# Optimization experiments

Hardware: AMD Instinct MI355X
Metric: run time of the kernel (lower is better)

## Reference

```python
import jax, jax.numpy as jnp
import numpy as np

BN_EPS = 1e-5

def _haar_details(x):
    # pywt.dwt2(x, 'haar') details for even H, W.
    # Block [[p, q], [r, s]] with p = x[2i,2j], q = x[2i,2j+1], r = x[2i+1,2j], s = x[2i+1,2j+1].
    # cH ('da'): detail along rows, approx along cols; cV ('ad'); cD ('dd').
    B, C, H, W = x.shape
    xb = x.reshape(B, C, H // 2, 2, W // 2, 2)
    p = xb[:, :, :, 0, :, 0]
    q = xb[:, :, :, 0, :, 1]
    r = xb[:, :, :, 1, :, 0]
    s = xb[:, :, :, 1, :, 1]
    cH = (p + q - r - s) * 0.5
    cV = (p - q + r - s) * 0.5
    cD = (p - q - r + s) * 0.5
    return cH, cV, cD

def setup_inputs() -> dict:
    key = jax.random.key(0)
    k1, k2 = jax.random.split(key)
    B, C, H, W = 8, 256, 128, 128
    x = jax.random.normal(k1, (B, C, H, W), dtype=jnp.float32)
    conv_w = jax.random.normal(k2, (C, 4 * C), dtype=jnp.float32) * (1.0 / np.sqrt(4 * C))
    gamma = jnp.ones((C,), dtype=jnp.float32)
    beta = jnp.zeros((C,), dtype=jnp.float32)
    return {"x": x, "conv_w": conv_w, "gamma": gamma, "beta": beta}

def reference(x, conv_w, gamma, beta):
    B, C, H, W = x.shape
    # Original detaches the wavelet branch (CPU numpy path) -> stop_gradient.
    xs = jax.lax.stop_gradient(x)
    cH, cV, cD = _haar_details(xs)
    # Bilinear upsample to (H, W); jax.image.resize bilinear == torch align_corners=False.
    up = lambda t: jax.image.resize(t, (B, C, H, W), method="bilinear")
    enhanced = jnp.concatenate([x, up(cH), up(cV), up(cD)], axis=1)  # [B, 4C, H, W]
    # 1x1 conv, no bias.
    y = jnp.einsum("bchw,oc->bohw", enhanced, conv_w)  # [B, C, H, W]
    # BatchNorm2d, training-mode (batch statistics, biased variance).
    mean = jnp.mean(y, axis=(0, 2, 3), keepdims=True)
    var = jnp.mean((y - mean) ** 2, axis=(0, 2, 3), keepdims=True)
    y_hat = (y - mean) * jax.lax.rsqrt(var + BN_EPS)
    out = jax.nn.relu(y_hat * gamma[None, :, None, None] + beta[None, :, None, None])
    return out
```

## Files before the change

### kernel.cpp

```cpp
#include <hip/hip_runtime.h>
#include <hip/hip_bf16.h>

typedef __bf16 bf16;
typedef __bf16 bf16x4 __attribute__((ext_vector_type(4)));
typedef __bf16 bf16x8 __attribute__((ext_vector_type(8)));
typedef float  f32x4  __attribute__((ext_vector_type(4)));

#define AS1 __attribute__((address_space(1)))
#define AS3 __attribute__((address_space(3)))

__device__ __forceinline__ void load16_to_lds(const bf16* g, bf16* l) {
    __builtin_amdgcn_global_load_lds((const AS1 unsigned int*)g,
                                     (AS3 unsigned int*)l, 16, 0, 0);
}

__global__ __launch_bounds__(256) void prep_w(const float* __restrict__ w,
                                              bf16* __restrict__ wb) {
    int idx = (blockIdx.x * 256 + threadIdx.x) * 4;
    const float4 v = *(const float4*)(w + idx);
    bf16x4 o; o[0]=(bf16)v.x; o[1]=(bf16)v.y; o[2]=(bf16)v.z; o[3]=(bf16)v.w;
    *(bf16x4*)(wb + idx) = o;
}

__device__ __forceinline__ int tix(int row, int chunk, int lo) {
    return row * 264 + (((chunk ^ ((row >> 2) & 7)) << 3) | lo);
}

__global__ __launch_bounds__(256, 2) void fused_x(const float* __restrict__ x,
                                                  const bf16* __restrict__ W,
                                                  bf16* __restrict__ cT,
                                                  bf16* __restrict__ y1) {
    __shared__ bf16 tile[64 * 264];
    const int bid = blockIdx.x;
    const int wt = bid & 3, j = (bid >> 2) & 63, b = bid >> 8;
    const int t = threadIdx.x;
    const int w0 = wt * 32;
    const int wave = t >> 6, lane = t & 63;
    const int quad = lane >> 4, l16 = lane & 15;
    const int wo = wave * 64;

    #pragma unroll
    for (int half = 0; half < 2; ++half) {
        float4 v[8];
        #pragma unroll
        for (int i = 0; i < 8; ++i) {
            int g = (half * 8 + i) * 256 + t;
            int c = g >> 4, rem = g & 15;
            int dlt = rem >> 3, w4 = rem & 7;
            v[i] = *(const float4*)(x +
                ((((size_t)b * 256 + c) * 128 + (2 * j + dlt)) * 128 + w0 + w4 * 4));
        }
        #pragma unroll
        for (int i = 0; i < 8; ++i) {
            int g = (half * 8 + i) * 256 + t;
            int c = g >> 4, rem = g & 15;
            int dlt = rem >> 3, w4 = rem & 7;
            int pos = dlt * 32 + w4 * 4;
            int cs = tix(pos, c >> 3, c & 7) - pos * 264;
            tile[(pos + 0) * 264 + cs] = (bf16)v[i].x;
            tile[(pos + 1) * 264 + cs] = (bf16)v[i].y;
            tile[(pos + 2) * 264 + cs] = (bf16)v[i].z;
            tile[(pos + 3) * 264 + cs] = (bf16)v[i].w;
        }
    }

    bf16x8 wf_cur[4], wf_nxt[4];
    #pragma unroll
    for (int jj = 0; jj < 4; ++jj)
        wf_cur[jj] = *(const bf16x8*)(W +
            (size_t)(wo + jj * 16 + l16) * 1024 + quad * 8);

    __syncthreads();

    #pragma unroll
    for (int i = 0; i < 2; ++i) {
        int q = i * 256 + t;
        int cq = q & 31, kc = q >> 5;
        bf16x8 vp = *(const bf16x8*)&tile[tix(2 * kc, cq, 0)];
        bf16x8 vq = *(const bf16x8*)&tile[tix(2 * kc + 1, cq, 0)];
        bf16x8 vr = *(const bf16x8*)&tile[tix(32 + 2 * kc, cq, 0)];
        bf16x8 vs = *(const bf16x8*)&tile[tix(33 + 2 * kc, cq, 0)];
        bf16x8 oh, ov, od;
        #pragma unroll
        for (int e = 0; e < 8; ++e) {
            float p = (float)vp[e], qq = (float)vq[e];
            float r = (float)vr[e], s = (float)vs[e];
            oh[e] = (bf16)(0.5f * (p + qq - r - s));
            ov[e] = (bf16)(0.5f * (p - qq + r - s));
            od[e] = (bf16)(0.5f * (p - qq - r + s));
        }
        size_t row = ((size_t)b * 4096 + j * 64 + wt * 16 + kc) * 768;
        *(bf16x8*)(cT + row + 0 * 256 + cq * 8) = oh;
        *(bf16x8*)(cT + row + 1 * 256 + cq * 8) = ov;
        *(bf16x8*)(cT + row + 2 * 256 + cq * 8) = od;
    }

    f32x4 acc[4][4] = {};
    #pragma unroll
    for (int kk = 0; kk < 256; kk += 32) {
        if (kk < 224) {
            #pragma unroll
            for (int jj = 0; jj < 4; ++jj)
                wf_nxt[jj] = *(const bf16x8*)(W +
                    (size_t)(wo + jj * 16 + l16) * 1024 + kk + 32 + quad * 8);
        }
        bf16x8 xf[4];
        #pragma unroll
        for (int i2 = 0; i2 < 4; ++i2)
            xf[i2] = *(const bf16x8*)&tile[tix(i2 * 16 + l16,
                                               (kk >> 3) + quad, 0)];
        #pragma unroll
        for (int i2 = 0; i2 < 4; ++i2)
            #pragma unroll
            for (int jj = 0; jj < 4; ++jj)
                acc[i2][jj] = __builtin_amdgcn_mfma_f32_16x16x32_bf16(
                    xf[i2], wf_cur[jj], acc[i2][jj], 0, 0, 0);
        #pragma unroll
        for (int jj = 0; jj < 4; ++jj) wf_cur[jj] = wf_nxt[jj];
    }

    #pragma unroll
    for (int i = 0; i < 4; ++i) {
        int p = i * 16 + quad * 4;
        int h = 2 * j + (p >> 5), wc = w0 + (p & 31);
        #pragma unroll
        for (int jj = 0; jj < 4; ++jj) {
            int o = wo + jj * 16 + l16;
            bf16x4 vv;
            #pragma unroll
            for (int r = 0; r < 4; ++r) vv[r] = (bf16)acc[i][jj][r];
            *(bf16x4*)(y1 + ((size_t)b * 256 + o) * 16384 + h * 128 + wc) = vv;
        }
    }
}

__global__ __launch_bounds__(256) void gemm2(const bf16* __restrict__ W,
                                             const bf16* __restrict__ cT,
                                             bf16* __restrict__ z) {
    __shared__ bf16 Xt[128 * 32];
    const int bid = blockIdx.x;
    const int m0 = (bid & 255) * 128, o0 = (bid >> 8) * 128;
    const int t = threadIdx.x;
    const int wave = t >> 6, lane = t & 63;
    const int quad = lane >> 4, l16 = lane & 15;
    const int wo = (wave >> 1) * 64, wm = (wave & 1) * 64;
    const int r_in = lane >> 2, cch = lane & 3;

    f32x4 acc[4][4] = {};
    const bf16* wbase = W + (size_t)o0 * 1024 + 256;
    const bf16* xbase = cT + (size_t)m0 * 768;

    bf16x8 af_cur[4], af_nxt[4];
    #pragma unroll
    for (int i = 0; i < 4; ++i)
        af_cur[i] = *(const bf16x8*)(wbase +
            (size_t)(wo + i * 16 + l16) * 1024 + quad * 8);

    for (int kk = 0; kk < 768; kk += 32) {
        #pragma unroll
        for (int i = 0; i < 2; ++i) {
            int rblk = wave * 2 + i;
            int row = rblk * 16 + r_in;
            load16_to_lds(xbase + (size_t)row * 768 + kk + cch * 8,
                          &Xt[rblk * 512 + lane * 8]);
        }
        __syncthreads();
        if (kk < 736) {
            #pragma unroll
            for (int i = 0; i < 4; ++i)
                af_nxt[i] = *(const bf16x8*)(wbase +
                    (size_t)(wo + i * 16 + l16) * 1024 + kk + 32 + quad * 8);
        }
        bf16x8 bfr[4];
        #pragma unroll
        for (int jj = 0; jj < 4; ++jj)
            bfr[jj] = *(const bf16x8*)&Xt[(wm + jj * 16 + l16) * 32 + quad * 8];
        #pragma unroll
        for (int i = 0; i < 4; ++i)
            #pragma unroll
            for (int jj = 0; jj < 4; ++jj)
                acc[i][jj] = __builtin_amdgcn_mfma_f32_16x16x32_bf16(
                    bfr[jj], af_cur[i], acc[i][jj], 0, 0, 0);
        __syncthreads();
        #pragma unroll
        for (int i = 0; i < 4; ++i) af_cur[i] = af_nxt[i];
    }

    #pragma unroll
    for (int i = 0; i < 4; ++i) {
        int o = o0 + wo + i * 16 + l16;
        #pragma unroll
        for (int jj = 0; jj < 4; ++jj) {
            int m = m0 + wm + jj * 16 + quad * 4;
            int bb = m >> 12, mp = m & 4095;
            bf16x4 vv;
            #pragma unroll
            for (int r = 0; r < 4; ++r) vv[r] = (bf16)acc[i][jj][r];
            *(bf16x4*)(z + ((size_t)bb * 256 + o) * 4096 + mp) = vv;
        }
    }
}

__device__ __forceinline__ void load_zplane(const bf16* zp, float* zs, int t) {
    for (int i = 0; i < 2; ++i) {
        int idx = (i * 256 + t) * 8;
        int j = idx >> 6, k = idx & 63;
        bf16x8 v = *(const bf16x8*)(zp + idx);
        #pragma unroll
        for (int e = 0; e < 8; ++e) zs[j * 65 + k + e] = (float)v[e];
    }
}

__device__ __forceinline__ void up8(const float* zs, int base, float* u) {
    int h = base >> 7, w0 = base & 127;
    int j0 = h >> 1;
    int jn = (h & 1) ? min(j0 + 1, 63) : max(j0 - 1, 0);
    int K = w0 >> 1;
    float z0[6], z1[6];
    #pragma unroll
    for (int d = 0; d < 6; ++d) {
        int kc = min(max(K - 1 + d, 0), 63);
        z0[d] = zs[j0 * 65 + kc];
        z1[d] = zs[jn * 65 + kc];
    }
    #pragma unroll
    for (int e = 0; e < 8; ++e) {
        int a = (e >> 1) + 1;
        int bb = (e & 1) ? a + 1 : a - 1;
        u[e] = 0.5625f * z0[a] + 0.1875f * (z0[bb] + z1[a]) + 0.0625f * z1[bb];
    }
}

__global__ __launch_bounds__(256) void stats_k(const bf16* __restrict__ y1,
                                               const bf16* __restrict__ z,
                                               float* __restrict__ stats) {
    __shared__ float zs[64 * 65];
    __shared__ float red[8];
    const int bid = blockIdx.x;
    const int o = bid & 255, b = bid >> 8;
    const int t = threadIdx.x;
    const bf16* zp = z + ((size_t)b * 256 + o) * 4096;
    const bf16* yp = y1 + ((size_t)b * 256 + o) * 16384;
    load_zplane(zp, zs, t);
    __syncthreads();
    float s = 0.f, ss = 0.f;
    for (int i = 0; i < 8; ++i) {
        int base = (i * 256 + t) * 8;
        float u[8];
        up8(zs, base, u);
        bf16x8 yv = *(const bf16x8*)(yp + base);
        #pragma unroll
        for (int e = 0; e < 8; ++e) {
            float y = (float)yv[e] + u[e];
            s += y; ss += y * y;
        }
    }
    #pragma unroll
    for (int off = 32; off > 0; off >>= 1) {
        s += __shfl_down(s, off);
        ss += __shfl_down(ss, off);
    }
    if ((t & 63) == 0) { red[t >> 6] = s; red[4 + (t >> 6)] = ss; }
    __syncthreads();
    if (t == 0) {
        atomicAdd(&stats[o],       red[0] + red[1] + red[2] + red[3]);
        atomicAdd(&stats[256 + o], red[4] + red[5] + red[6] + red[7]);
    }
}

__global__ __launch_bounds__(256) void apply_k(const bf16* __restrict__ y1,
                                               const bf16* __restrict__ z,
                                               const float* __restrict__ stats,
                                               const float* __restrict__ gamma,
                                               const float* __restrict__ beta,
                                               float* __restrict__ out) {
    __shared__ float zs[64 * 65];
    const int bid = blockIdx.x;
    const int o = bid & 255, b = bid >> 8;
    const int t = threadIdx.x;
    const bf16* zp = z + ((size_t)b * 256 + o) * 4096;
    const bf16* yp = y1 + ((size_t)b * 256 + o) * 16384;
    float* op = out + ((size_t)b * 256 + o) * 16384;
    const float n = 131072.f;
    float mean = stats[o] / n;
    float var = stats[256 + o] / n - mean * mean;
    float sc = rsqrtf(var + 1e-5f) * gamma[o];
    float sh = beta[o] - mean * sc;
    load_zplane(zp, zs, t);
    __syncthreads();
    for (int i = 0; i < 8; ++i) {
        int base = (i * 256 + t) * 8;
        float u[8];
        up8(zs, base, u);
        bf16x8 yv = *(const bf16x8*)(yp + base);
        float4 o0, o1;
        o0.x = fmaxf(fmaf((float)yv[0] + u[0], sc, sh), 0.f);
        o0.y = fmaxf(fmaf((float)yv[1] + u[1], sc, sh), 0.f);
        o0.z = fmaxf(fmaf((float)yv[2] + u[2], sc, sh), 0.f);
        o0.w = fmaxf(fmaf((float)yv[3] + u[3], sc, sh), 0.f);
        o1.x = fmaxf(fmaf((float)yv[4] + u[4], sc, sh), 0.f);
        o1.y = fmaxf(fmaf((float)yv[5] + u[5], sc, sh), 0.f);
        o1.z = fmaxf(fmaf((float)yv[6] + u[6], sc, sh), 0.f);
        o1.w = fmaxf(fmaf((float)yv[7] + u[7], sc, sh), 0.f);
        *(float4*)(op + base) = o0;
        *(float4*)(op + base + 4) = o1;
    }
}

extern "C" void kernel_launch(void* const* d_in, const int* in_sizes, int n_in,
                              void* d_out, int out_size, void* d_ws, size_t ws_size,
                              hipStream_t stream) {
    const float* x      = (const float*)d_in[0];
    const float* conv_w = (const float*)d_in[1];
    const float* gamma  = (const float*)d_in[2];
    const float* beta   = (const float*)d_in[3];
    float* out = (float*)d_out;

    char* ws = (char*)d_ws;
    bf16*  Wbf   = (bf16*)ws;
    bf16*  z     = (bf16*)(ws + (512ll << 10));
    float* stats = (float*)(ws + (512ll << 10) + (16ll << 20));
    bf16*  cT    = (bf16*)(ws + (512ll << 10) + (16ll << 20) + 4096);
    bf16*  y1    = (bf16*)(ws + (512ll << 10) + (64ll << 20) + 4096);

    hipMemsetAsync(stats, 0, 4096, stream);
    prep_w<<<256, 256, 0, stream>>>(conv_w, Wbf);
    fused_x<<<2048, 256, 0, stream>>>(x, Wbf, cT, y1);
    gemm2<<<512, 256, 0, stream>>>(Wbf, cT, z);
    stats_k<<<2048, 256, 0, stream>>>(y1, z, stats);
    apply_k<<<2048, 256, 0, stream>>>(y1, z, stats, gamma, beta, out);
}
```

Baseline: 347.6 us.

## Fold Haar transform into weights and fuse detail GEMM into main kernel

The Haar detail coefficients are linear in the four pixels p,q,r,s, so prep_w now combines the three detail weight blocks into four per-tap weight blocks. fused_x then computes the low-resolution z directly from the LDS tile with an extra K=1024 MFMA loop. This removes the separate cT buffer write/read and the gemm2 launch. In exchange each block does extra low-occupancy MFMA work using a single 16-row fragment per wave, and the LDS tile writes were rewritten as vectorised bf16x8 stores.

```diff
diff --git a/kernel.cpp b/kernel.cpp
--- a/kernel.cpp
+++ b/kernel.cpp
@@ -6,20 +6,17 @@
 typedef __bf16 bf16x8 __attribute__((ext_vector_type(8)));
 typedef float  f32x4  __attribute__((ext_vector_type(4)));
 
-#define AS1 __attribute__((address_space(1)))
-#define AS3 __attribute__((address_space(3)))
-
-__device__ __forceinline__ void load16_to_lds(const bf16* g, bf16* l) {
-    __builtin_amdgcn_global_load_lds((const AS1 unsigned int*)g,
-                                     (AS3 unsigned int*)l, 16, 0, 0);
-}
-
 __global__ __launch_bounds__(256) void prep_w(const float* __restrict__ w,
                                               bf16* __restrict__ wb) {
-    int idx = (blockIdx.x * 256 + threadIdx.x) * 4;
-    const float4 v = *(const float4*)(w + idx);
-    bf16x4 o; o[0]=(bf16)v.x; o[1]=(bf16)v.y; o[2]=(bf16)v.z; o[3]=(bf16)v.w;
-    *(bf16x4*)(wb + idx) = o;
+    const int o = blockIdx.x, c = threadIdx.x;
+    const float* wr = w + o * 1024;
+    const float w1 = wr[c], w2 = wr[256 + c], w3 = wr[512 + c], w4 = wr[768 + c];
+    bf16* wo_ = wb + o * 1280;
+    wo_[c]              = (bf16)w1;
+    wo_[256 + 0*256 + c] = (bf16)(0.5f * ( w2 + w3 + w4));
+    wo_[256 + 1*256 + c] = (bf16)(0.5f * ( w2 - w3 - w4));
+    wo_[256 + 2*256 + c] = (bf16)(0.5f * (-w2 + w3 - w4));
+    wo_[256 + 3*256 + c] = (bf16)(0.5f * (-w2 - w3 + w4));
 }
 
 __device__ __forceinline__ int tix(int row, int chunk, int lo) {
@@ -28,7 +25,7 @@
 
 __global__ __launch_bounds__(256, 2) void fused_x(const float* __restrict__ x,
                                                   const bf16* __restrict__ W,
-                                                  bf16* __restrict__ cT,
+                                                  bf16* __restrict__ z,
                                                   bf16* __restrict__ y1) {
     __shared__ bf16 tile[64 * 264];
     const int bid = blockIdx.x;
@@ -40,27 +37,24 @@
     const int wo = wave * 64;
 
     #pragma unroll
-    for (int half = 0; half < 2; ++half) {
+    for (int it = 0; it < 2; ++it) {
+        const int a   = it * 256 + t;
+        const int c8  = a >> 4;
+        const int p4  = a & 15;
+        const int dlt = p4 >> 3, w4 = p4 & 7;
+        const float* xp = x + (((size_t)b * 256 + c8 * 8) * 128 + (2*j + dlt)) * 128
+                            + w0 + w4 * 4;
         float4 v[8];
         #pragma unroll
-        for (int i = 0; i < 8; ++i) {
-            int g = (half * 8 + i) * 256 + t;
-            int c = g >> 4, rem = g & 15;
-            int dlt = rem >> 3, w4 = rem & 7;
-            v[i] = *(const float4*)(x +
-                ((((size_t)b * 256 + c) * 128 + (2 * j + dlt)) * 128 + w0 + w4 * 4));
-        }
-        #pragma unroll
-        for (int i = 0; i < 8; ++i) {
-            int g = (half * 8 + i) * 256 + t;
-            int c = g >> 4, rem = g & 15;
-            int dlt = rem >> 3, w4 = rem & 7;
-            int pos = dlt * 32 + w4 * 4;
-            int cs = tix(pos, c >> 3, c & 7) - pos * 264;
-            tile[(pos + 0) * 264 + cs] = (bf16)v[i].x;
-            tile[(pos + 1) * 264 + cs] = (bf16)v[i].y;
-            tile[(pos + 2) * 264 + cs] = (bf16)v[i].z;
-            tile[(pos + 3) * 264 + cs] = (bf16)v[i].w;
+        for (int i = 0; i < 8; ++i)
+            v[i] = *(const float4*)(xp + (size_t)i * 16384);
+        #pragma unroll
+        for (int e = 0; e < 4; ++e) {
+            bf16x8 o8;
+            #pragma unroll
+            for (int i = 0; i < 8; ++i) o8[i] = (bf16)((&v[i].x)[e]);
+            const int pos = dlt * 32 + w4 * 4 + e;
+            *(bf16x8*)&tile[tix(pos, c8, 0)] = o8;
         }
     }
 
@@ -68,32 +62,9 @@
     #pragma unroll
     for (int jj = 0; jj < 4; ++jj)
         wf_cur[jj] = *(const bf16x8*)(W +
-            (size_t)(wo + jj * 16 + l16) * 1024 + quad * 8);
-
-    __syncthreads();
-
-    #pragma unroll
-    for (int i = 0; i < 2; ++i) {
-        int q = i * 256 + t;
-        int cq = q & 31, kc = q >> 5;
-        bf16x8 vp = *(const bf16x8*)&tile[tix(2 * kc, cq, 0)];
-        bf16x8 vq = *(const bf16x8*)&tile[tix(2 * kc + 1, cq, 0)];
-        bf16x8 vr = *(const bf16x8*)&tile[tix(32 + 2 * kc, cq, 0)];
-        bf16x8 vs = *(const bf16x8*)&tile[tix(33 + 2 * kc, cq, 0)];
-        bf16x8 oh, ov, od;
-        #pragma unroll
-        for (int e = 0; e < 8; ++e) {
-            float p = (float)vp[e], qq = (float)vq[e];
-            float r = (float)vr[e], s = (float)vs[e];
-            oh[e] = (bf16)(0.5f * (p + qq - r - s));
-            ov[e] = (bf16)(0.5f * (p - qq + r - s));
-            od[e] = (bf16)(0.5f * (p - qq - r + s));
-        }
-        size_t row = ((size_t)b * 4096 + j * 64 + wt * 16 + kc) * 768;
-        *(bf16x8*)(cT + row + 0 * 256 + cq * 8) = oh;
-        *(bf16x8*)(cT + row + 1 * 256 + cq * 8) = ov;
-        *(bf16x8*)(cT + row + 2 * 256 + cq * 8) = od;
-    }
+            (size_t)(wo + jj * 16 + l16) * 1280 + quad * 8);
+
+    __syncthreads();
 
     f32x4 acc[4][4] = {};
     #pragma unroll
@@ -102,7 +73,12 @@
             #pragma unroll
             for (int jj = 0; jj < 4; ++jj)
                 wf_nxt[jj] = *(const bf16x8*)(W +
-                    (size_t)(wo + jj * 16 + l16) * 1024 + kk + 32 + quad * 8);
+                    (size_t)(wo + jj * 16 + l16) * 1280 + kk + 32 + quad * 8);
+        } else {
+            #pragma unroll
+            for (int jj = 0; jj < 4; ++jj)
+                wf_nxt[jj] = *(const bf16x8*)(W +
+                    (size_t)(wo + jj * 16 + l16) * 1280 + 256 + quad * 8);
         }
         bf16x8 xf[4];
         #pragma unroll
@@ -119,6 +95,27 @@
         for (int jj = 0; jj < 4; ++jj) wf_cur[jj] = wf_nxt[jj];
     }
 
+    f32x4 acc2[4] = {};
+    #pragma unroll
+    for (int kz = 0; kz < 1024; kz += 32) {
+        if (kz < 992) {
+            #pragma unroll
+            for (int jj = 0; jj < 4; ++jj)
+                wf_nxt[jj] = *(const bf16x8*)(W +
+                    (size_t)(wo + jj * 16 + l16) * 1280 + 256 + kz + 32 + quad * 8);
+        }
+        const int tap  = kz >> 8;
+        const int trow = ((tap >> 1) << 5) | (tap & 1);
+        const bf16x8 af = *(const bf16x8*)&tile[tix(trow + 2 * l16,
+                                                    ((kz & 255) >> 3) + quad, 0)];
+        #pragma unroll
+        for (int jj = 0; jj < 4; ++jj)
+            acc2[jj] = __builtin_amdgcn_mfma_f32_16x16x32_bf16(
+                af, wf_cur[jj], acc2[jj], 0, 0, 0);
+        #pragma unroll
+        for (int jj = 0; jj < 4; ++jj) wf_cur[jj] = wf_nxt[jj];
+    }
+
     #pragma unroll
     for (int i = 0; i < 4; ++i) {
         int p = i * 16 + quad * 4;
@@ -132,72 +129,14 @@
             *(bf16x4*)(y1 + ((size_t)b * 256 + o) * 16384 + h * 128 + wc) = vv;
         }
     }
-}
-
-__global__ __launch_bounds__(256) void gemm2(const bf16* __restrict__ W,
-                                             const bf16* __restrict__ cT,
-                                             bf16* __restrict__ z) {
-    __shared__ bf16 Xt[128 * 32];
-    const int bid = blockIdx.x;
-    const int m0 = (bid & 255) * 128, o0 = (bid >> 8) * 128;
-    const int t = threadIdx.x;
-    const int wave = t >> 6, lane = t & 63;
-    const int quad = lane >> 4, l16 = lane & 15;
-    const int wo = (wave >> 1) * 64, wm = (wave & 1) * 64;
-    const int r_in = lane >> 2, cch = lane & 3;
-
-    f32x4 acc[4][4] = {};
-    const bf16* wbase = W + (size_t)o0 * 1024 + 256;
-    const bf16* xbase = cT + (size_t)m0 * 768;
-
-    bf16x8 af_cur[4], af_nxt[4];
-    #pragma unroll
-    for (int i = 0; i < 4; ++i)
-        af_cur[i] = *(const bf16x8*)(wbase +
-            (size_t)(wo + i * 16 + l16) * 1024 + quad * 8);
-
-    for (int kk = 0; kk < 768; kk += 32) {
-        #pragma unroll
-        for (int i = 0; i < 2; ++i) {
-            int rblk = wave * 2 + i;
-            int row = rblk * 16 + r_in;
-            load16_to_lds(xbase + (size_t)row * 768 + kk + cch * 8,
-                          &Xt[rblk * 512 + lane * 8]);
-        }
-        __syncthreads();
-        if (kk < 736) {
-            #pragma unroll
-            for (int i = 0; i < 4; ++i)
-                af_nxt[i] = *(const bf16x8*)(wbase +
-                    (size_t)(wo + i * 16 + l16) * 1024 + kk + 32 + quad * 8);
-        }
-        bf16x8 bfr[4];
-        #pragma unroll
-        for (int jj = 0; jj < 4; ++jj)
-            bfr[jj] = *(const bf16x8*)&Xt[(wm + jj * 16 + l16) * 32 + quad * 8];
-        #pragma unroll
-        for (int i = 0; i < 4; ++i)
-            #pragma unroll
-            for (int jj = 0; jj < 4; ++jj)
-                acc[i][jj] = __builtin_amdgcn_mfma_f32_16x16x32_bf16(
-                    bfr[jj], af_cur[i], acc[i][jj], 0, 0, 0);
-        __syncthreads();
-        #pragma unroll
-        for (int i = 0; i < 4; ++i) af_cur[i] = af_nxt[i];
-    }
-
-    #pragma unroll
-    for (int i = 0; i < 4; ++i) {
-        int o = o0 + wo + i * 16 + l16;
-        #pragma unroll
-        for (int jj = 0; jj < 4; ++jj) {
-            int m = m0 + wm + jj * 16 + quad * 4;
-            int bb = m >> 12, mp = m & 4095;
-            bf16x4 vv;
-            #pragma unroll
-            for (int r = 0; r < 4; ++r) vv[r] = (bf16)acc[i][jj][r];
-            *(bf16x4*)(z + ((size_t)bb * 256 + o) * 4096 + mp) = vv;
-        }
+
+    #pragma unroll
+    for (int jj = 0; jj < 4; ++jj) {
+        int o = wo + jj * 16 + l16;
+        bf16x4 vv;
+        #pragma unroll
+        for (int r = 0; r < 4; ++r) vv[r] = (bf16)acc2[jj][r];
+        *(bf16x4*)(z + ((size_t)b * 256 + o) * 4096 + j * 64 + wt * 16 + quad * 4) = vv;
     }
 }
 
@@ -318,15 +257,13 @@
 
     char* ws = (char*)d_ws;
     bf16*  Wbf   = (bf16*)ws;
-    bf16*  z     = (bf16*)(ws + (512ll << 10));
-    float* stats = (float*)(ws + (512ll << 10) + (16ll << 20));
-    bf16*  cT    = (bf16*)(ws + (512ll << 10) + (16ll << 20) + 4096);
-    bf16*  y1    = (bf16*)(ws + (512ll << 10) + (64ll << 20) + 4096);
+    bf16*  z     = (bf16*)(ws + (1ll << 20));
+    float* stats = (float*)(ws + (17ll << 20));
+    bf16*  y1    = (bf16*)(ws + (17ll << 20) + (1ll << 16));
 
     hipMemsetAsync(stats, 0, 4096, stream);
     prep_w<<<256, 256, 0, stream>>>(conv_w, Wbf);
-    fused_x<<<2048, 256, 0, stream>>>(x, Wbf, cT, y1);
-    gemm2<<<512, 256, 0, stream>>>(Wbf, cT, z);
+    fused_x<<<2048, 256, 0, stream>>>(x, Wbf, z, y1);
     stats_k<<<2048, 256, 0, stream>>>(y1, z, stats);
     apply_k<<<2048, 256, 0, stream>>>(y1, z, stats, gamma, beta, out);
 }
```

Result: slower. 428.8 us (+23.3%).
